# Optimization experiments

Measured on AMD Instinct MI355X. Metric: run time of the kernel, lower is better.

Reference implementation:

```python
import jax, jax.numpy as jnp
import numpy as np

D = 128           # volume / particle box size (pixels)
B = 8             # particles per batch
K = 125           # SO(3) grid poses (5x5x5 around each center Euler)
TOPK = 2          # keep_top_k_values
MAX_SHIFT_FRAC = 0.25  # main_config.projmatching.max_shift_fraction


def setup_inputs() -> dict:
    key = jax.random.key(0)
    k1, k2, k3, k4 = jax.random.split(key, 4)
    vol = jax.random.normal(k1, (D, D, D), dtype=jnp.float32)
    parts = jax.random.normal(k2, (B, D, D), dtype=jnp.float32)
    ctf = jax.random.uniform(k3, (B, D, D // 2 + 1), dtype=jnp.float32)
    euler_degs = jax.random.normal(k4, (K, 3), dtype=jnp.float32) * 8.0
    return {"vol": vol, "parts": parts, "ctf": ctf, "euler_degs": euler_degs}


def _rot_z(t):
    c, s = jnp.cos(t), jnp.sin(t)
    z, o = jnp.zeros_like(t), jnp.ones_like(t)
    return jnp.stack([jnp.stack([c, -s, z], -1),
                      jnp.stack([s, c, z], -1),
                      jnp.stack([z, z, o], -1)], -2)


def _rot_y(t):
    c, s = jnp.cos(t), jnp.sin(t)
    z, o = jnp.zeros_like(t), jnp.ones_like(t)
    return jnp.stack([jnp.stack([c, z, s], -1),
                      jnp.stack([z, o, z], -1),
                      jnp.stack([-s, z, c], -1)], -2)


def euler_zyz_to_matrix(degs):
    # RELION Euler convention ZYZ: R = Rz(a) @ Ry(b) @ Rz(c)
    rad = jnp.deg2rad(degs)
    return _rot_z(rad[..., 0]) @ _rot_y(rad[..., 1]) @ _rot_z(rad[..., 2])


def trilinear_sample(vol, zi, yi, xi):
    # vol: (Dz, Dy, W) complex64; coords: (K, h, w) float32 array indices
    Dz, Dy, W = vol.shape
    z0, y0, x0 = jnp.floor(zi), jnp.floor(yi), jnp.floor(xi)
    tz, ty, tx = zi - z0, yi - y0, xi - x0
    out = jnp.zeros(zi.shape, dtype=vol.dtype)
    for dz in (0, 1):
        wz = tz if dz else 1.0 - tz
        zc = z0 + dz
        vz = (zc >= 0) & (zc < Dz)
        zdx = jnp.clip(zc, 0, Dz - 1).astype(jnp.int32)
        for dy in (0, 1):
            wy = ty if dy else 1.0 - ty
            yc = y0 + dy
            vy = (yc >= 0) & (yc < Dy)
            ydx = jnp.clip(yc, 0, Dy - 1).astype(jnp.int32)
            for dx in (0, 1):
                wx = tx if dx else 1.0 - tx
                xc = x0 + dx
                vx = (xc >= 0) & (xc < W)
                xdx = jnp.clip(xc, 0, W - 1).astype(jnp.int32)
                w = jnp.where(vz & vy & vx, wz * wy * wx, 0.0)
                out = out + w * vol[zdx, ydx, xdx]
    return out


def project_fourier(vol_rfft, rotmats):
    # extract_central_slices_rfft: pose-dependent gather+trilinear interp of a
    # central slice from the fftshifted 3D rfft volume. Output: (K, D, D//2+1).
    d = D
    w = d // 2 + 1
    y = jnp.arange(d, dtype=jnp.float32) - d // 2   # fftshifted full-dim freqs (pixel units)
    x = jnp.arange(w, dtype=jnp.float32)            # rfft (non-negative) freqs
    yy, xx = jnp.meshgrid(y, x, indexing='ij')      # (d, w)
    coords = jnp.stack([xx, yy, jnp.zeros_like(yy)], -1)       # xyz, (d, w, 3), z = 0 plane
    rot = jnp.einsum('kij,hwj->khwi', rotmats, coords)          # (K, d, w, 3) rotated xyz
    conj_mask = rot[..., 0] < 0                                  # Hermitian symmetry: flip to x>=0 half
    rot = jnp.where(conj_mask[..., None], -rot, rot)
    xi = rot[..., 0]
    yi = rot[..., 1] + d // 2
    zi = rot[..., 2] + d // 2
    samples = trilinear_sample(vol_rfft, zi, yi, xi)
    samples = jnp.where(conj_mask, jnp.conj(samples), samples)
    r2 = xx ** 2 + yy ** 2                                       # zero beyond Nyquist radius
    samples = jnp.where(r2[None] > (d // 2) ** 2, 0.0, samples)
    return samples


def reference(vol, parts, ctf, euler_degs):
    # compute_dft: rfft volume, fftshift non-rfft dims
    vol_rfft = jnp.fft.fftshift(jnp.fft.rfftn(vol), axes=(0, 1))
    parts_rfft = jnp.fft.fftshift(jnp.fft.rfft2(parts), axes=(-2,))  # (B, D, W)
    rotmats = euler_zyz_to_matrix(euler_degs)                        # (K, 3, 3)
    projs = project_fourier(vol_rfft, rotmats)                       # (K, D, W)
    projs = ctf[:, None] * projs[None]                               # _apply_ctfF: (B, K, D, W)
    # correlate_dft_2d: cross-correlation via iFFT of parts * conj(projs)
    prod = parts_rfft[:, None] * jnp.conj(projs)
    prod = jnp.fft.ifftshift(prod, axes=(-2,))
    corr = jnp.fft.irfft2(prod, s=(D, D))                            # (B, K, D, D)
    corr = jnp.fft.fftshift(corr, axes=(-2, -1))                     # zero shift at center
    # _extract_ccor_max: restrict to |shift| <= max_shift_fraction*D, take top-k peaks
    center = D // 2
    max_shift = int(MAX_SHIFT_FRAC * D)
    idx = jnp.arange(D) - center
    win = (jnp.abs(idx)[:, None] <= max_shift) & (jnp.abs(idx)[None, :] <= max_shift)
    masked = jnp.where(win, corr, -jnp.inf)
    flat = masked.reshape(B, K, D * D)
    vals, top_idx = jax.lax.top_k(flat, TOPK)                        # (B, K, TOPK)
    shifts = jnp.stack([top_idx // D - center, top_idx % D - center], -1)  # (B, K, TOPK, 2) yx
    return vals, shifts
```

## Files before the change

### kernel.cpp

```cpp
#include <hip/hip_runtime.h>
#include <math.h>

#define D 128
#define W 65
#define NK 125
#define NB 8
#define SLAB (D*W)
#define TWO_PI 6.28318530717958647692f
#define R2C 0.70710678118654752440f
#define C8C 0.92387953251128675613f
#define S8C 0.38268343236508977173f
#define ARS 146
#define GS  67
#define BRS 68


__device__ __forceinline__ bool better(float va, int ia, float vb, int ib) {
    return (va > vb) || (va == vb && ia < ib);
}
__device__ __forceinline__ float2 cmul(float2 a, float2 b) {
    return make_float2(a.x*b.x - a.y*b.y, a.x*b.y + a.y*b.x);
}
__device__ __forceinline__ void cmac(float2& acc, float2 a, float2 b) {
    acc.x = fmaf(a.x, b.x, fmaf(-a.y, b.y, acc.x));
    acc.y = fmaf(a.x, b.y, fmaf( a.y, b.x, acc.y));
}
__device__ __forceinline__ float2 cadd(float2 a, float2 b){ return make_float2(a.x+b.x, a.y+b.y); }
__device__ __forceinline__ float2 csub(float2 a, float2 b){ return make_float2(a.x-b.x, a.y-b.y); }

__device__ __forceinline__ void fft8_fwd(const float2* x, float2* a) {
    float2 e0 = x[0], o0 = x[1], e1 = x[2], o1 = x[3];
    float2 e2 = x[4], o2 = x[5], e3 = x[6], o3 = x[7];
    float2 t0 = cadd(e0, e2), t1 = csub(e0, e2);
    float2 t2 = cadd(e1, e3), t3 = csub(e1, e3);
    float2 E0 = cadd(t0, t2), E2 = csub(t0, t2);
    float2 E1 = make_float2(t1.x + t3.y, t1.y - t3.x);
    float2 E3 = make_float2(t1.x - t3.y, t1.y + t3.x);
    float2 u0 = cadd(o0, o2), u1 = csub(o0, o2);
    float2 u2 = cadd(o1, o3), u3 = csub(o1, o3);
    float2 O0 = cadd(u0, u2), O2 = csub(u0, u2);
    float2 O1 = make_float2(u1.x + u3.y, u1.y - u3.x);
    float2 O3 = make_float2(u1.x - u3.y, u1.y + u3.x);
    float2 w1 = make_float2(R2C*(O1.x + O1.y), R2C*(O1.y - O1.x));
    float2 w2 = make_float2(O2.y, -O2.x);
    float2 w3 = make_float2(R2C*(O3.y - O3.x), -R2C*(O3.x + O3.y));
    a[0] = cadd(E0, O0); a[4] = csub(E0, O0);
    a[1] = cadd(E1, w1); a[5] = csub(E1, w1);
    a[2] = cadd(E2, w2); a[6] = csub(E2, w2);
    a[3] = cadd(E3, w3); a[7] = csub(E3, w3);
}

__device__ __forceinline__ void ifft8_reg(const float2* x, float2* a) {
    float2 e0 = x[0], o0 = x[1], e1 = x[2], o1 = x[3];
    float2 e2 = x[4], o2 = x[5], e3 = x[6], o3 = x[7];
    float2 t0 = cadd(e0, e2), t1 = csub(e0, e2);
    float2 t2 = cadd(e1, e3), t3 = csub(e1, e3);
    float2 E0 = cadd(t0, t2), E2 = csub(t0, t2);
    float2 E1 = make_float2(t1.x - t3.y, t1.y + t3.x);
    float2 E3 = make_float2(t1.x + t3.y, t1.y - t3.x);
    float2 u0 = cadd(o0, o2), u1 = csub(o0, o2);
    float2 u2 = cadd(o1, o3), u3 = csub(o1, o3);
    float2 O0 = cadd(u0, u2), O2 = csub(u0, u2);
    float2 O1 = make_float2(u1.x - u3.y, u1.y + u3.x);
    float2 O3 = make_float2(u1.x + u3.y, u1.y - u3.x);
    float2 w1o = make_float2(R2C*(O1.x - O1.y), R2C*(O1.x + O1.y));
    float2 w2o = make_float2(-O2.y, O2.x);
    float2 w3o = make_float2(R2C*(-O3.x - O3.y), R2C*(O3.x - O3.y));
    a[0] = cadd(E0, O0); a[4] = csub(E0, O0);
    a[1] = cadd(E1, w1o); a[5] = csub(E1, w1o);
    a[2] = cadd(E2, w2o); a[6] = csub(E2, w2o);
    a[3] = cadd(E3, w3o); a[7] = csub(E3, w3o);
}


template<int MODE>
__device__ __forceinline__ void fft128v2(const float* __restrict__ inf,
                                         const float2* __restrict__ inc,
                                         float2* __restrict__ out,
                                         const float* __restrict__ ct,
                                         int l0, int nlines,
                                         float2* __restrict__ Fl,
                                         float2* __restrict__ twf) {
    int tid = threadIdx.x;
    int line, t;
    if (MODE == 0) { t = tid & 7; line = tid >> 3; }
    else           { line = tid & 31; t = tid >> 5; }
    int l = l0 + line;
    bool live = (l < nlines);

    if (tid < 128) {
        float s, c;
        sincosf(-TWO_PI * (float)tid / 128.0f, &s, &c);
        twf[tid] = make_float2(c, s);
    }

    int base = 0, stride = 1;
    if (MODE == 1 || MODE == 4) { base = (l / W) * SLAB + (l % W); stride = W; }
    else if (MODE == 2) { base = l; stride = SLAB; }

    float2 xe[8], xo[8];
    if (live) {
        if (MODE == 0) {
            const float* r = inf + (size_t)l * D;
            #pragma unroll
            for (int j = 0; j < 8; ++j) {
                xe[j] = make_float2(r[t + 16*j], 0.f);
                xo[j] = make_float2(r[t + 8 + 16*j], 0.f);
            }
        } else {
            #pragma unroll
            for (int j = 0; j < 8; ++j) {
                xe[j] = inc[base + (t + 16*j) * stride];
                xo[j] = inc[base + (t + 8 + 16*j) * stride];
            }
        }
    } else {
        #pragma unroll
        for (int j = 0; j < 8; ++j) { xe[j] = make_float2(0,0); xo[j] = make_float2(0,0); }
    }
    float2 E[8], O[8];
    fft8_fwd(xe, E);
    fft8_fwd(xo, O);
    {
        const float2 w16[8] = {
            { 1.f, 0.f }, { C8C, -S8C }, { R2C, -R2C }, { S8C, -C8C },
            { 0.f, -1.f }, { -S8C, -C8C }, { -R2C, -R2C }, { -C8C, -S8C }
        };
        float2* Fp = Fl + line * 137 + t * 17;
        #pragma unroll
        for (int kk = 0; kk < 8; ++kk) {
            float2 wo = cmul(w16[kk], O[kk]);
            Fp[kk]     = cadd(E[kk], wo);
            Fp[kk + 8] = csub(E[kk], wo);
        }
    }
    __syncthreads();
    if (live) {
        const float2* Fr = Fl + line * 137;
        #pragma unroll
        for (int half = 0; half < 2; ++half) {
            int kk = t + 8 * half;
            float2 Gv[8];
            #pragma unroll
            for (int tt = 0; tt < 8; ++tt) {
                Gv[tt] = cmul(Fr[tt * 17 + kk], twf[(tt * kk) & 127]);
            }
            float2 o[8];
            fft8_fwd(Gv, o);
            if (MODE == 0) {
                #pragma unroll
                for (int s = 0; s < 8; ++s) {
                    int kf = kk + 16 * s;
                    if (kf <= 64) out[(size_t)l * W + kf] = o[s];
                }
            } else {
                #pragma unroll
                for (int s = 0; s < 8; ++s) {
                    int slot = (kk + 16 * s) ^ 64;
                    if (MODE == 4) {
                        float cf = ct[(size_t)l * D + slot];
                        out[(size_t)l * D + slot] = make_float2(o[s].x * cf, o[s].y * cf);
                    } else {
                        out[base + slot * stride] = o[s];
                    }
                }
            }
        }
    }
}


__global__ __launch_bounds__(256) void k1_kernel(const float* __restrict__ vol,
                                                 const float* __restrict__ parts,
                                                 const float* __restrict__ ctf,
                                                 const float* __restrict__ euler,
                                                 float2* __restrict__ bufA,
                                                 float2* __restrict__ pT1,
                                                 float* __restrict__ CT,
                                                 float* __restrict__ rot) {
    __shared__ float2 Fl[32 * 137];
    __shared__ float2 twf[128];
    int bid = blockIdx.x;
    int tid = threadIdx.x;
    if (bid < 512) {
        fft128v2<0>(vol, nullptr, bufA, nullptr, bid * 32, D*D, Fl, twf);
    } else if (bid < 544) {
        fft128v2<0>(parts, nullptr, pT1, nullptr, (bid - 512) * 32, NB*D, Fl, twf);
    } else if (bid == 544) {
        int k = tid;
        if (k < NK) {
            const float d2r = 0.017453292519943295f;
            float a = euler[k*3+0]*d2r, b = euler[k*3+1]*d2r, c = euler[k*3+2]*d2r;
            float sa, ca, sb, cb, sc, cc;
            sincosf(a, &sa, &ca); sincosf(b, &sb, &cb); sincosf(c, &sc, &cc);
            rot[k*9+0] =  ca*cb*cc - sa*sc;
            rot[k*9+1] = -ca*cb*sc - sa*cc;
            rot[k*9+2] =  ca*sb;
            rot[k*9+3] =  sa*cb*cc + ca*sc;
            rot[k*9+4] = -sa*cb*sc + ca*cc;
            rot[k*9+5] =  sa*sb;
            rot[k*9+6] = -sb*cc;
            rot[k*9+7] =  sb*sc;
            rot[k*9+8] =  cb;
        }
    } else {
        int i = (bid - 545) * 256 + tid;
        if (i < NB * W * D) {
            int m = i & (D-1);
            int t2 = i >> 7;
            int x = t2 % W;
            int b = t2 / W;
            CT[i] = ctf[b * SLAB + m * W + x];
        }
    }
}

__global__ __launch_bounds__(256) void k2_kernel(const float2* __restrict__ bufA,
                                                 float2* __restrict__ bufB,
                                                 const float2* __restrict__ pT1,
                                                 float2* __restrict__ ST,
                                                 const float* __restrict__ CT) {
    __shared__ float2 Fl[32 * 137];
    __shared__ float2 twf[128];
    int bid = blockIdx.x;
    if (bid < 260) fft128v2<1>(nullptr, bufA, bufB, nullptr, bid * 32, D*W, Fl, twf);
    else           fft128v2<4>(nullptr, pT1, ST, CT, (bid - 260) * 32, NB*W, Fl, twf);
}

__global__ __launch_bounds__(256) void k3_kernel(const float2* __restrict__ bufB,
                                                 float2* __restrict__ bufA) {
    __shared__ float2 Fl[32 * 137];
    __shared__ float2 twf[128];
    fft128v2<2>(nullptr, bufB, bufA, nullptr, blockIdx.x * 32, SLAB, Fl, twf);
}


__global__ __launch_bounds__(256) void proj_kernel(const float2* __restrict__ vol,
                                                   const float* __restrict__ rot,
                                                   float2* __restrict__ projT) {
    int bid = blockIdx.x;
    int xcd = bid & 7, ii = bid >> 3;
    int wg = (xcd < 7) ? (xcd * 508 + ii) : (3556 + ii);
    int idx = wg * 256 + threadIdx.x;
    if (idx >= NK * D * W) return;
    int h = idx & (D-1);
    int t2 = idx >> 7;
    int w = t2 % W;
    int k = t2 / W;
    int yy = h - 64;
    if (w*w + yy*yy > 4096) { projT[idx] = make_float2(0.f, 0.f); return; }
    float x = (float)w;
    float y = (float)yy;
    const float* R = rot + k*9;
    float rx = R[0]*x + R[1]*y;
    float ry = R[3]*x + R[4]*y;
    float rz = R[6]*x + R[7]*y;
    bool neg = rx < 0.0f;
    if (neg) { rx = -rx; ry = -ry; rz = -rz; }
    float xi = rx;
    float yi = ry + 64.0f;
    float zi = rz + 64.0f;
    float z0 = floorf(zi), y0 = floorf(yi), x0 = floorf(xi);
    float tz = zi - z0, ty = yi - y0, tx = xi - x0;
    int z0i = (int)z0, y0i = (int)y0, x0i = (int)x0;
    float ar = 0.f, ai = 0.f;
    for (int dz = 0; dz < 2; ++dz) {
        float wz = dz ? tz : 1.0f - tz;
        int zc = z0i + dz;
        bool vz = (zc >= 0) && (zc < D);
        int zx = min(max(zc, 0), D-1);
        for (int dy = 0; dy < 2; ++dy) {
            float wy = dy ? ty : 1.0f - ty;
            int yc = y0i + dy;
            bool vy = (yc >= 0) && (yc < D);
            int yx = min(max(yc, 0), D-1);
            for (int dx = 0; dx < 2; ++dx) {
                float wx = dx ? tx : 1.0f - tx;
                int xc = x0i + dx;
                bool vx = (xc >= 0) && (xc < W);
                int xx = min(max(xc, 0), W-1);
                float wt = (vz && vy && vx) ? wz*wy*wx : 0.0f;
                float2 v = vol[zx * SLAB + yx * W + xx];
                ar = fmaf(wt, v.x, ar);
                ai = fmaf(wt, v.y, ai);
            }
        }
    }
    if (neg) ai = -ai;
    projT[idx] = make_float2(ar, ai);
}


__global__ __launch_bounds__(256, 3) void corr_kernel(const float2* __restrict__ ST,
                                                      const float2* __restrict__ PJT,
                                                      float* __restrict__ outv) {
    __shared__ float2 tw[128];
    __shared__ __align__(16) float2 AbBC[17*ARS];
    __shared__ float2 Gs[17*GS];
    __shared__ float  Ny[65];
    __shared__ float  redv[8];
    __shared__ int    redi[8];

    int g = blockIdx.x;
    int logical = (g & 7) * 125 + (g >> 3);
    int k = logical >> 3;
    int b = logical & 7;
    int tid = threadIdx.x;
    const float inv_d = 1.0f / 128.0f;

    if (tid < 128) {
        float s, c;
        sincosf(TWO_PI * (float)tid / 128.0f, &s, &c);
        tw[tid] = make_float2(c, s);
    }

    const float2* Sb = ST + b * (W * D);
    const float2* Jk = PJT + k * (W * D);

    int lane = tid & 63;
    int wv = tid >> 6;
    int sv = lane & 7;
    int vp = (96 + lane) & 127;
    float acc[16];
    #pragma unroll
    for (int j = 0; j < 16; ++j) acc[j] = 0.0f;
    float accR = 0.0f;
    int ur = 0, vr = 0;
    if (tid < 129) { if (tid < 65) { ur = 64; vr = tid; } else { ur = tid - 65; vr = 64; } }

    __syncthreads();

    float2 wvp = tw[vp];
    float2 tq = make_float2(1.0f, 0.0f);

    for (int cg = 0; cg < 4; ++cg) {
        {
            int lim1 = (cg == 0) ? 17 * 16 : 16 * 16;
            for (int i = tid; i < lim1; i += 256) {
                int l = i >> 4, m0 = i & 15;
                int x = (l < 16) ? (4*cg + (l >> 2) + 16 * (l & 3)) : 64;
                const float2* Sx = Sb + x * 128 + m0;
                const float2* Jx = Jk + x * 128 + m0;
                float2 p[8];
                #pragma unroll
                for (int j = 0; j < 8; ++j) {
                    float2 s = Sx[16*j];
                    float2 pj = Jx[16*j];
                    p[j] = make_float2(s.x*pj.x + s.y*pj.y, s.y*pj.x - s.x*pj.y);
                }
                float2 A[8];
                ifft8_reg(p, A);
                float2* dst = AbBC + l * ARS + m0;
                dst[0] = A[0];
                #pragma unroll
                for (int r = 1; r < 8; ++r) dst[r*18] = cmul(A[r], tw[(r * m0) & 127]);
            }
        }
        __syncthreads();
        {
            int lim2 = (cg == 0) ? 136 : 128;
            for (int i = tid; i < lim2; i += 256) {
                int l, r;
                if (i < 128) { l = i & 15; r = i >> 4; }
                else         { l = 16; r = i - 128; }
                const float4* Ar = (const float4*)(AbBC + l * ARS + r * 18);
                float2 xe[8], xo[8];
                #pragma unroll
                for (int j = 0; j < 8; ++j) {
                    float4 a = Ar[j];
                    xe[j] = make_float2(a.x, a.y);
                    xo[j] = make_float2(a.z, a.w);
                }
                float2 E[8], O[8];
                ifft8_reg(xe, E);
                ifft8_reg(xo, O);
                const float2 w16p[8] = {
                    { 1.f, 0.f }, { C8C, S8C }, { R2C, R2C }, { S8C, C8C },
                    { 0.f, 1.f }, { -S8C, C8C }, { -R2C, R2C }, { -C8C, S8C }
                };
                float2* Gl = Gs + l * GS;
                #pragma unroll
                for (int t = 0; t < 8; ++t) {
                    float2 wo = cmul(w16p[t], O[t]);
                    float2 lowv  = cadd(E[t], wo);
                    float2 highv = csub(E[t], wo);
                    int klow = r + 8*t;
                    if (t <= 3) Gl[klow + 32] = lowv;
                    if (t == 4 && r == 0) Gl[64] = lowv;
                    if (t >= 4) Gl[klow - 32] = highv;
                }
            }
        }
        __syncthreads();
        {
            float2* BC = AbBC;
            int lim = (cg == 0) ? 325 : 260;
            for (int i = tid; i < lim; i += 256) {
                if (i < 260) {
                    int q = i / 65;
                    int u2 = i - q * 65;
                    float sg = (u2 & 1) ? -inv_d : inv_d;
                    const float2* Gq = Gs + (4*q) * GS + u2;
                    float2 h0 = Gq[0*GS];
                    float2 h1 = Gq[1*GS];
                    float2 h2 = Gq[2*GS];
                    float2 h3 = Gq[3*GS];
                    h0.x *= sg; h0.y *= sg; h1.x *= sg; h1.y *= sg;
                    h2.x *= sg; h2.y *= sg; h3.x *= sg; h3.y *= sg;
                    if (cg == 0 && q == 0) { h0.x *= 0.5f; h0.y *= 0.5f; }
                    const float sc = 2.0f * inv_d;
                    float2 p1 = make_float2(R2C*(h1.x - h1.y), R2C*(h1.x + h1.y));
                    float2 q1 = make_float2(R2C*(-h1.x - h1.y), R2C*(h1.x - h1.y));
                    float2 i1 = make_float2(-h1.y, h1.x);
                    float2 i2 = make_float2(-h2.y, h2.x);
                    float2 n2 = make_float2( h2.y, -h2.x);
                    float2 p3 = make_float2(R2C*(h3.x - h3.y), R2C*(h3.x + h3.y));
                    float2 q3 = make_float2(R2C*(-h3.x - h3.y), R2C*(h3.x - h3.y));
                    float2 i3 = make_float2(-h3.y, h3.x);
                    float2 a02 = cadd(h0, h2), s02 = csub(h0, h2);
                    float2 s0 = cadd(a02, cadd(h1, h3));
                    float2 s4 = csub(a02, cadd(h1, h3));
                    float2 s2 = cadd(s02, csub(i1, i3));
                    float2 s6 = csub(s02, csub(i1, i3));
                    float2 b0i = cadd(h0, i2);
                    float2 b0n = cadd(h0, n2);
                    float2 s1 = cadd(b0i, cadd(p1, q3));
                    float2 s5 = csub(b0i, cadd(p1, q3));
                    float2 s3 = cadd(b0n, cadd(q1, p3));
                    float2 s7 = csub(b0n, cadd(q1, p3));
                    float2* Bp = BC + q * (8*BRS) + u2;
                    Bp[0*BRS] = make_float2(s0.x*sc, s0.y*sc);
                    Bp[1*BRS] = make_float2(s1.x*sc, s1.y*sc);
                    Bp[2*BRS] = make_float2(s2.x*sc, s2.y*sc);
                    Bp[3*BRS] = make_float2(s3.x*sc, s3.y*sc);
                    Bp[4*BRS] = make_float2(s4.x*sc, s4.y*sc);
                    Bp[5*BRS] = make_float2(s5.x*sc, s5.y*sc);
                    Bp[6*BRS] = make_float2(s6.x*sc, s6.y*sc);
                    Bp[7*BRS] = make_float2(s7.x*sc, s7.y*sc);
                } else {
                    int u2 = i - 260;
                    Ny[u2] = ((u2 & 1) ? -inv_d : inv_d) * Gs[16*GS + u2].x;
                }
            }
        }
        __syncthreads();
        {
            #pragma unroll
            for (int q = 0; q < 4; ++q) {
                const float4* Bq = (const float4*)(AbBC + q * (8*BRS) + sv * BRS + wv * 16);
                float tx = tq.x, ty = tq.y;
                #pragma unroll
                for (int jp = 0; jp < 8; ++jp) {
                    float4 bb = Bq[jp];
                    acc[2*jp]   = fmaf(bb.x, tx, fmaf(-bb.y, ty, acc[2*jp]));
                    acc[2*jp+1] = fmaf(bb.z, tx, fmaf(-bb.w, ty, acc[2*jp+1]));
                }
                tq = cmul(tq, wvp);
            }
            if (cg == 0) {
                float sgn = (lane & 1) ? -inv_d : inv_d;
                #pragma unroll
                for (int j = 0; j < 16; ++j) acc[j] = fmaf(sgn, Ny[wv * 16 + j], acc[j]);
            }
            if (tid < 129) {
                int sr = vr & 7;
                int vpr = (96 + vr) & 127;
                float a = accR;
                #pragma unroll
                for (int q = 0; q < 4; ++q) {
                    float2 t = tw[((4*cg + q) * vpr) & 127];
                    float2 bv = AbBC[q * (8*BRS) + sr * BRS + ur];
                    a = fmaf(bv.x, t.x, fmaf(-bv.y, t.y, a));
                }
                if (cg == 0) a += (vr & 1) ? -inv_d * Ny[ur] : inv_d * Ny[ur];
                accR = a;
            }
        }
        __syncthreads();
    }

    float v1 = -INFINITY, v2 = -INFINITY;
    int i1 = 0x7fffffff, i2 = 0x7fffffff;
    #pragma unroll
    for (int j = 0; j < 16; ++j) {
        float val = acc[j];
        int uu = wv * 16 + j;
        int fl = (32 + uu) * D + (32 + lane);
        if (better(val, fl, v1, i1)) { v2 = v1; i2 = i1; v1 = val; i1 = fl; }
        else if (better(val, fl, v2, i2)) { v2 = val; i2 = fl; }
    }
    if (tid < 129) {
        int fl = (32 + ur) * D + (32 + vr);
        if (better(accR, fl, v1, i1)) { v2 = v1; i2 = i1; v1 = accR; i1 = fl; }
        else if (better(accR, fl, v2, i2)) { v2 = accR; i2 = fl; }
    }
    for (int off = 32; off > 0; off >>= 1) {
        float b1 = __shfl_down(v1, off); int j1 = __shfl_down(i1, off);
        float b2 = __shfl_down(v2, off); int j2 = __shfl_down(i2, off);
        if (better(b1, j1, v1, i1)) {
            float nv2; int ni2;
            if (better(v1, i1, b2, j2)) { nv2 = v1; ni2 = i1; } else { nv2 = b2; ni2 = j2; }
            v1 = b1; i1 = j1; v2 = nv2; i2 = ni2;
        } else {
            if (better(b1, j1, v2, i2)) { v2 = b1; i2 = j1; }
        }
    }
    int wave = tid >> 6;
    if ((tid & 63) == 0) {
        redv[wave*2]   = v1; redi[wave*2]   = i1;
        redv[wave*2+1] = v2; redi[wave*2+1] = i2;
    }
    __syncthreads();
    if (tid == 0) {
        float r1 = -INFINITY, r2 = -INFINITY;
        int q1 = 0x7fffffff, q2 = 0x7fffffff;
        for (int i = 0; i < 8; ++i) {
            float val = redv[i]; int fl = redi[i];
            if (better(val, fl, r1, q1)) { r2 = r1; q2 = q1; r1 = val; q1 = fl; }
            else if (better(val, fl, r2, q2)) { r2 = val; q2 = fl; }
        }
        int base = (b * NK + k) * 2;
        outv[base]     = r1;
        outv[base + 1] = r2;
        float* os = outv + NB*NK*2;
        os[(base    )*2 + 0] = (float)(q1 / D - 64);
        os[(base    )*2 + 1] = (float)(q1 % D - 64);
        os[(base + 1)*2 + 0] = (float)(q2 / D - 64);
        os[(base + 1)*2 + 1] = (float)(q2 % D - 64);
    }
}


extern "C" void kernel_launch(void* const* d_in, const int* in_sizes, int n_in,
                              void* d_out, int out_size, void* d_ws, size_t ws_size,
                              hipStream_t stream) {
    const float* vol   = (const float*)d_in[0];
    const float* parts = (const float*)d_in[1];
    const float* ctf   = (const float*)d_in[2];
    const float* euler = (const float*)d_in[3];
    float* out = (float*)d_out;

    const int VOLC = D * SLAB;
    float2* bufA   = (float2*)d_ws;
    float2* bufB   = bufA + VOLC;
    float2* pT1    = bufB + VOLC;
    float2* ST     = pT1 + NB * SLAB;
    float2* PJT    = ST + NB * W * D;
    float*  CT     = (float*)(PJT + NK * W * D);
    float*  rot    = CT + NB * W * D;

    k1_kernel<<<805, 256, 0, stream>>>(vol, parts, ctf, euler, bufA, pT1, CT, rot);
    k2_kernel<<<277, 256, 0, stream>>>(bufA, bufB, pT1, ST, CT);
    k3_kernel<<<260, 256, 0, stream>>>(bufB, bufA);
    proj_kernel<<<4063, 256, 0, stream>>>(bufA, rot, PJT);
    corr_kernel<<<NB * NK, 256, 0, stream>>>(ST, PJT, out);
}
```

Before: 75.29 us.

## Pack two (batch, pose) correlation problems per 512-thread block

The correlation kernel now runs 512-thread blocks, each handling two (b,k) pairs with separate shared-memory halves. The block count drops from 1000 to 500, and the XCD-aware index remap is adjusted to match. Per-thread twiddle factors for the first FFT stage are hoisted into registers instead of being re-read from shared memory. This removes per-block setup such as twiddle sincos and reduces block-scheduling overhead. In exchange, shared memory per block doubles, the two halves are coupled through block-wide barriers, and the launch bounds change.

```diff
diff --git a/kernel.cpp b/kernel.cpp
--- a/kernel.cpp
+++ b/kernel.cpp
@@ -291,21 +291,25 @@
 }
 
 
-__global__ __launch_bounds__(256, 3) void corr_kernel(const float2* __restrict__ ST,
+__global__ __launch_bounds__(512, 4) void corr_kernel(const float2* __restrict__ ST,
                                                       const float2* __restrict__ PJT,
                                                       float* __restrict__ outv) {
     __shared__ float2 tw[128];
-    __shared__ __align__(16) float2 AbBC[17*ARS];
-    __shared__ float2 Gs[17*GS];
-    __shared__ float  Ny[65];
-    __shared__ float  redv[8];
-    __shared__ int    redi[8];
-
+    __shared__ __align__(16) float2 AbBC2[2][17*ARS];
+    __shared__ float2 Gs2[2][17*GS];
+    __shared__ float  Ny2[2][65];
+    __shared__ float  redv[16];
+    __shared__ int    redi[16];
+
+    int tid = threadIdx.x;
+    int half = tid >> 8;
+    int t = tid & 255;
     int g = blockIdx.x;
-    int logical = (g & 7) * 125 + (g >> 3);
-    int k = logical >> 3;
-    int b = logical & 7;
-    int tid = threadIdx.x;
+    int xcd = g & 7, ii = g >> 3;
+    int L = (xcd < 4) ? (xcd * 63 + ii) : (252 + (xcd - 4) * 62 + ii);
+    int pair = 2 * L + half;
+    int k = pair >> 3;
+    int b = pair & 7;
     const float inv_d = 1.0f / 128.0f;
 
     if (tid < 128) {
@@ -314,11 +318,15 @@
         tw[tid] = make_float2(c, s);
     }
 
+    float2* AbBC = AbBC2[half];
+    float2* Gs   = Gs2[half];
+    float*  Ny   = Ny2[half];
+
     const float2* Sb = ST + b * (W * D);
     const float2* Jk = PJT + k * (W * D);
 
-    int lane = tid & 63;
-    int wv = tid >> 6;
+    int lane = t & 63;
+    int wv = t >> 6;
     int sv = lane & 7;
     int vp = (96 + lane) & 127;
     float acc[16];
@@ -326,17 +334,23 @@
     for (int j = 0; j < 16; ++j) acc[j] = 0.0f;
     float accR = 0.0f;
     int ur = 0, vr = 0;
-    if (tid < 129) { if (tid < 65) { ur = 64; vr = tid; } else { ur = tid - 65; vr = 64; } }
+    if (t < 129) { if (t < 65) { ur = 64; vr = t; } else { ur = t - 65; vr = 64; } }
 
     __syncthreads();
 
     float2 wvp = tw[vp];
     float2 tq = make_float2(1.0f, 0.0f);
+
+    int m01 = t & 15;
+    float2 twr[8];
+    twr[0] = make_float2(1.f, 0.f);
+    #pragma unroll
+    for (int r = 1; r < 8; ++r) twr[r] = tw[(r * m01) & 127];
 
     for (int cg = 0; cg < 4; ++cg) {
         {
             int lim1 = (cg == 0) ? 17 * 16 : 16 * 16;
-            for (int i = tid; i < lim1; i += 256) {
+            for (int i = t; i < lim1; i += 256) {
                 int l = i >> 4, m0 = i & 15;
                 int x = (l < 16) ? (4*cg + (l >> 2) + 16 * (l & 3)) : 64;
                 const float2* Sx = Sb + x * 128 + m0;
@@ -353,13 +367,13 @@
                 float2* dst = AbBC + l * ARS + m0;
                 dst[0] = A[0];
                 #pragma unroll
-                for (int r = 1; r < 8; ++r) dst[r*18] = cmul(A[r], tw[(r * m0) & 127]);
+                for (int r = 1; r < 8; ++r) dst[r*18] = cmul(A[r], twr[r]);
             }
         }
         __syncthreads();
         {
             int lim2 = (cg == 0) ? 136 : 128;
-            for (int i = tid; i < lim2; i += 256) {
+            for (int i = t; i < lim2; i += 256) {
                 int l, r;
                 if (i < 128) { l = i & 15; r = i >> 4; }
                 else         { l = 16; r = i - 128; }
@@ -380,14 +394,14 @@
                 };
                 float2* Gl = Gs + l * GS;
                 #pragma unroll
-                for (int t = 0; t < 8; ++t) {
-                    float2 wo = cmul(w16p[t], O[t]);
-                    float2 lowv  = cadd(E[t], wo);
-                    float2 highv = csub(E[t], wo);
-                    int klow = r + 8*t;
-                    if (t <= 3) Gl[klow + 32] = lowv;
-                    if (t == 4 && r == 0) Gl[64] = lowv;
-                    if (t >= 4) Gl[klow - 32] = highv;
+                for (int tt = 0; tt < 8; ++tt) {
+                    float2 wo = cmul(w16p[tt], O[tt]);
+                    float2 lowv  = cadd(E[tt], wo);
+                    float2 highv = csub(E[tt], wo);
+                    int klow = r + 8*tt;
+                    if (tt <= 3) Gl[klow + 32] = lowv;
+                    if (tt == 4 && r == 0) Gl[64] = lowv;
+                    if (tt >= 4) Gl[klow - 32] = highv;
                 }
             }
         }
@@ -395,7 +409,7 @@
         {
             float2* BC = AbBC;
             int lim = (cg == 0) ? 325 : 260;
-            for (int i = tid; i < lim; i += 256) {
+            for (int i = t; i < lim; i += 256) {
                 if (i < 260) {
                     int q = i / 65;
                     int u2 = i - q * 65;
@@ -462,15 +476,15 @@
                 #pragma unroll
                 for (int j = 0; j < 16; ++j) acc[j] = fmaf(sgn, Ny[wv * 16 + j], acc[j]);
             }
-            if (tid < 129) {
+            if (t < 129) {
                 int sr = vr & 7;
                 int vpr = (96 + vr) & 127;
                 float a = accR;
                 #pragma unroll
                 for (int q = 0; q < 4; ++q) {
-                    float2 t = tw[((4*cg + q) * vpr) & 127];
+                    float2 tt = tw[((4*cg + q) * vpr) & 127];
                     float2 bv = AbBC[q * (8*BRS) + sr * BRS + ur];
-                    a = fmaf(bv.x, t.x, fmaf(-bv.y, t.y, a));
+                    a = fmaf(bv.x, tt.x, fmaf(-bv.y, tt.y, a));
                 }
                 if (cg == 0) a += (vr & 1) ? -inv_d * Ny[ur] : inv_d * Ny[ur];
                 accR = a;
@@ -489,7 +503,7 @@
         if (better(val, fl, v1, i1)) { v2 = v1; i2 = i1; v1 = val; i1 = fl; }
         else if (better(val, fl, v2, i2)) { v2 = val; i2 = fl; }
     }
-    if (tid < 129) {
+    if (t < 129) {
         int fl = (32 + ur) * D + (32 + vr);
         if (better(accR, fl, v1, i1)) { v2 = v1; i2 = i1; v1 = accR; i1 = fl; }
         else if (better(accR, fl, v2, i2)) { v2 = accR; i2 = fl; }
@@ -511,11 +525,11 @@
         redv[wave*2+1] = v2; redi[wave*2+1] = i2;
     }
     __syncthreads();
-    if (tid == 0) {
+    if (t == 0) {
         float r1 = -INFINITY, r2 = -INFINITY;
         int q1 = 0x7fffffff, q2 = 0x7fffffff;
         for (int i = 0; i < 8; ++i) {
-            float val = redv[i]; int fl = redi[i];
+            float val = redv[half*8 + i]; int fl = redi[half*8 + i];
             if (better(val, fl, r1, q1)) { r2 = r1; q2 = q1; r1 = val; q1 = fl; }
             else if (better(val, fl, r2, q2)) { r2 = val; q2 = fl; }
         }
@@ -553,5 +567,5 @@
     k2_kernel<<<277, 256, 0, stream>>>(bufA, bufB, pT1, ST, CT);
     k3_kernel<<<260, 256, 0, stream>>>(bufB, bufA);
     proj_kernel<<<4063, 256, 0, stream>>>(bufA, rot, PJT);
-    corr_kernel<<<NB * NK, 256, 0, stream>>>(ST, PJT, out);
-}
+    corr_kernel<<<500, 512, 0, stream>>>(ST, PJT, out);
+}
```

New measurement: 75.76 us. About the same (+0.6%).
